# Performance work log

Hardware: AMD Instinct MI355X
Metric: run time of the kernel (lower is better)

## Reference

```python
import jax, jax.numpy as jnp
import numpy as np

TOP_K = 2
NORM_P = 1  # moe_normalize_expert_weights


def setup_inputs() -> dict:
    key = jax.random.key(0)
    k1, k2 = jax.random.split(key)
    B, S, H, E = 4, 4096, 4096, 64
    x = jax.random.normal(k1, (B, S, H), dtype=jnp.float32)
    # Linear(H, E, bias=False) weight, torch layout [E, H]
    W = jax.random.normal(k2, (E, H), dtype=jnp.float32) * (1.0 / np.sqrt(H))
    return {"x": x, "W": W}


def reference(x, W):
    H = x.shape[-1]
    xt = x.reshape(-1, H)                      # [T, H]
    logits = jnp.einsum('th,eh->te', xt, W)    # [T, E]
    scores = jax.nn.softmax(logits, axis=-1)   # [T, E]
    expert_weights, expert_indices = jax.lax.top_k(scores, TOP_K)  # [T, K]
    # p=1 norm over the selected weights (values are positive post-softmax)
    norm = jnp.sum(jnp.abs(expert_weights), axis=-1, keepdims=True)
    expert_weights = expert_weights / norm
    return scores, expert_weights, expert_indices
```

## Files before the change

kernel.cpp:

```cpp
#include <hip/hip_runtime.h>
#include <math.h>

#define TOKS  16384
#define HD    4096
#define NE    64
#define MT    32
#define KT    64
#define NTHR  256
#define NTILE (HD / KT)

typedef unsigned int   u32;
typedef unsigned short u16;
typedef short v8s __attribute__((ext_vector_type(8)));
typedef float v4f __attribute__((ext_vector_type(4)));

__device__ __forceinline__ void split2(float a, float b, u32& hi, u32& lo) {
    u32 ua = __float_as_uint(a), ub = __float_as_uint(b);
    hi = (ub & 0xffff0000u) | (ua >> 16);
    float la = a - __uint_as_float(ua & 0xffff0000u);
    float lb = b - __uint_as_float(ub & 0xffff0000u);
    lo = (__float_as_uint(lb) & 0xffff0000u) | (__float_as_uint(la) >> 16);
}

__global__ __launch_bounds__(256) void wsplit_kernel(const float* __restrict__ W,
                                                     char* __restrict__ wsd) {
    const int gid = blockIdx.x * 256 + threadIdx.x;
    const float4 f = ((const float4*)W)[gid];
    const int idx = gid << 2;
    const int e   = idx >> 12;
    const int col = idx & 4095;
    const int k   = col >> 6;
    const int j   = col & 63;
    u32 h0, h1, l0, l1;
    split2(f.x, f.y, h0, l0);
    split2(f.z, f.w, h1, l1);
    char* base = wsd + ((size_t)k << 14) + (e << 7) + ((j << 1) ^ ((e & 7) << 4));
    *(uint2*)(base)        = make_uint2(h0, h1);
    *(uint2*)(base + 8192) = make_uint2(l0, l1);
}

#define GLDS(G, L)                                                             \
    __builtin_amdgcn_global_load_lds(                                          \
        (const __attribute__((address_space(1))) u32*)(G),                     \
        (__attribute__((address_space(3))) u32*)(L), 16, 0, 0)

__global__ __launch_bounds__(NTHR, 2) void router_kernel(
    const float* __restrict__ x, const char* __restrict__ wsd,
    float* __restrict__ scores, float* __restrict__ wout, float* __restrict__ iout)
{
    __shared__ __align__(16) u16 WT[2][8192];
    __shared__ float Ls[MT][NE + 1];
    __shared__ float Ssum[MT], Smax[MT];

    const int t    = threadIdx.x;
    const int tok0 = blockIdx.x * MT;
    const int lane = t & 63;
    const int w    = t >> 6;
    const int wt   = w & 1;
    const int weh  = w >> 1;
    const int q    = lane >> 4, r = lane & 15;
    const int arow  = wt * 16 + r;
    const int brow0 = weh * 32 + r;
    const int brow1 = weh * 32 + 16 + r;

    const float* xrow = x + (size_t)(tok0 + arow) * HD;
    const int qe = q * 8;

    const int sw0 = (brow0 & 7) << 4;
    const int sw1 = (brow1 & 7) << 4;
    const int ob0h = brow0 * 128, ob0l = 8192 + ob0h;
    const int ob1h = brow1 * 128, ob1l = 8192 + ob1h;
    const int q16 = q * 16;
    const int c00 = ob0h + ((q16)      ^ sw0);
    const int c01 = ob0h + ((64 + q16) ^ sw0);
    const int d00 = ob0l + ((q16)      ^ sw0);
    const int d01 = ob0l + ((64 + q16) ^ sw0);
    const int c10 = ob1h + ((q16)      ^ sw1);
    const int c11 = ob1h + ((64 + q16) ^ sw1);
    const int d10 = ob1l + ((q16)      ^ sw1);
    const int d11 = ob1l + ((64 + q16) ^ sw1);

    const char* wsl = wsd + w * 4096 + lane * 16;

    v4f acc0 = {0.f, 0.f, 0.f, 0.f};
    v4f acc1 = {0.f, 0.f, 0.f, 0.f};

    float4 a0A, a1A, a2A, a3A, a0B, a1B, a2B, a3B;

#define XLOAD(S, T)                                                 \
    do { const float* xp = xrow + (T) * KT + qe;                    \
         a0##S = *(const float4*)(xp);                              \
         a1##S = *(const float4*)(xp + 4);                          \
         a2##S = *(const float4*)(xp + 32);                         \
         a3##S = *(const float4*)(xp + 36); } while (0)

#define STAGE_W(T, B)                                               \
    do { const char* gs = wsl + ((size_t)(T) << 14);                \
         char* ls = ((char*)&WT[B][0]) + w * 4096;                  \
         GLDS(gs,        ls);                                       \
         GLDS(gs + 1024, ls + 1024);                                \
         GLDS(gs + 2048, ls + 2048);                                \
         GLDS(gs + 3072, ls + 3072); } while (0)

#define COMPUTE(S, B)                                                            \
    do {                                                                         \
        const char* WB = (const char*)&WT[B][0];                                 \
        union { v8s v; u32 u[4]; } ah, al;                                       \
        v8s bh0, bl0, bh1, bl1;                                                  \
                                                                      \
        split2(a0##S.x, a0##S.y, ah.u[0], al.u[0]);                              \
        split2(a0##S.z, a0##S.w, ah.u[1], al.u[1]);                              \
        split2(a1##S.x, a1##S.y, ah.u[2], al.u[2]);                              \
        split2(a1##S.z, a1##S.w, ah.u[3], al.u[3]);                              \
        bh0 = *(const v8s*)(WB + c00); bl0 = *(const v8s*)(WB + d00);            \
        bh1 = *(const v8s*)(WB + c10); bl1 = *(const v8s*)(WB + d10);            \
        acc0 = __builtin_amdgcn_mfma_f32_16x16x32_bf16(ah.v, bh0, acc0, 0, 0, 0);\
        acc0 = __builtin_amdgcn_mfma_f32_16x16x32_bf16(al.v, bh0, acc0, 0, 0, 0);\
        acc0 = __builtin_amdgcn_mfma_f32_16x16x32_bf16(ah.v, bl0, acc0, 0, 0, 0);\
        acc1 = __builtin_amdgcn_mfma_f32_16x16x32_bf16(ah.v, bh1, acc1, 0, 0, 0);\
        acc1 = __builtin_amdgcn_mfma_f32_16x16x32_bf16(al.v, bh1, acc1, 0, 0, 0);\
        acc1 = __builtin_amdgcn_mfma_f32_16x16x32_bf16(ah.v, bl1, acc1, 0, 0, 0);\
                                                                      \
        split2(a2##S.x, a2##S.y, ah.u[0], al.u[0]);                              \
        split2(a2##S.z, a2##S.w, ah.u[1], al.u[1]);                              \
        split2(a3##S.x, a3##S.y, ah.u[2], al.u[2]);                              \
        split2(a3##S.z, a3##S.w, ah.u[3], al.u[3]);                              \
        bh0 = *(const v8s*)(WB + c01); bl0 = *(const v8s*)(WB + d01);            \
        bh1 = *(const v8s*)(WB + c11); bl1 = *(const v8s*)(WB + d11);            \
        acc0 = __builtin_amdgcn_mfma_f32_16x16x32_bf16(ah.v, bh0, acc0, 0, 0, 0);\
        acc0 = __builtin_amdgcn_mfma_f32_16x16x32_bf16(al.v, bh0, acc0, 0, 0, 0);\
        acc0 = __builtin_amdgcn_mfma_f32_16x16x32_bf16(ah.v, bl0, acc0, 0, 0, 0);\
        acc1 = __builtin_amdgcn_mfma_f32_16x16x32_bf16(ah.v, bh1, acc1, 0, 0, 0);\
        acc1 = __builtin_amdgcn_mfma_f32_16x16x32_bf16(al.v, bh1, acc1, 0, 0, 0);\
        acc1 = __builtin_amdgcn_mfma_f32_16x16x32_bf16(ah.v, bl1, acc1, 0, 0, 0);\
    } while (0)

    XLOAD(A, 0);
    STAGE_W(0, 0);
    __syncthreads();

    for (int tt = 0; tt < NTILE; tt += 2) {
        STAGE_W(tt + 1, 1);
        XLOAD(B, tt + 1);
        COMPUTE(A, 0);
        __syncthreads();
        if (tt + 2 < NTILE) {
            STAGE_W(tt + 2, 0);
            XLOAD(A, tt + 2);
        }
        COMPUTE(B, 1);
        __syncthreads();
    }

#pragma unroll
    for (int reg = 0; reg < 4; ++reg) {
        Ls[wt * 16 + q * 4 + reg][weh * 32 + r]      = acc0[reg];
        Ls[wt * 16 + q * 4 + reg][weh * 32 + 16 + r] = acc1[reg];
    }
    __syncthreads();

    {
        const int tk = t >> 3;
        const int sl = t & 7;
        float m = -3.402823466e+38f;
#pragma unroll
        for (int j = 0; j < 8; ++j) m = fmaxf(m, Ls[tk][sl + 8 * j]);
#pragma unroll
        for (int d = 1; d < 8; d <<= 1) m = fmaxf(m, __shfl_xor(m, d, 64));

        float s = 0.f, v1 = -1.f, v2 = -1.f;
        int   i1 = 0, i2 = 0;
#pragma unroll
        for (int j = 0; j < 8; ++j) {
            const int e = sl + 8 * j;
            const float ex = expf(Ls[tk][e] - m);
            s += ex;
            if (ex > v1)      { v2 = v1; i2 = i1; v1 = ex; i1 = e; }
            else if (ex > v2) { v2 = ex; i2 = e; }
        }
#pragma unroll
        for (int d = 1; d < 8; d <<= 1) {
            const float ov1 = __shfl_xor(v1, d, 64);
            const int   oi1 = __shfl_xor(i1, d, 64);
            const float ov2 = __shfl_xor(v2, d, 64);
            const int   oi2 = __shfl_xor(i2, d, 64);
            s += __shfl_xor(s, d, 64);
            if (ov1 > v1 || (ov1 == v1 && oi1 < i1)) {
                if (ov2 > v1 || (ov2 == v1 && oi2 < i1)) { v2 = ov2; i2 = oi2; }
                else                                     { v2 = v1;  i2 = i1;  }
                v1 = ov1; i1 = oi1;
            } else if (ov1 > v2 || (ov1 == v2 && oi1 < i2)) {
                v2 = ov1; i2 = oi1;
            }
        }
        if (sl == 0) {
            const float s1 = v1 / s, s2 = v2 / s;
            const float ws_ = s1 + s2;
            wout[(size_t)(tok0 + tk) * 2 + 0] = s1 / ws_;
            wout[(size_t)(tok0 + tk) * 2 + 1] = s2 / ws_;
            iout[(size_t)(tok0 + tk) * 2 + 0] = (float)i1;
            iout[(size_t)(tok0 + tk) * 2 + 1] = (float)i2;
            Ssum[tk] = s;
            Smax[tk] = m;
        }
    }
    __syncthreads();

#pragma unroll
    for (int it = 0; it < (MT * NE) / NTHR; ++it) {
        const int f  = it * NTHR + t;
        const int tk = f >> 6, e = f & 63;
        scores[(size_t)(tok0 + tk) * NE + e] = expf(Ls[tk][e] - Smax[tk]) / Ssum[tk];
    }
}

extern "C" void kernel_launch(void* const* d_in, const int* in_sizes, int n_in,
                              void* d_out, int out_size, void* d_ws, size_t ws_size,
                              hipStream_t stream) {
    (void)in_sizes; (void)n_in; (void)out_size; (void)ws_size;
    const float* x = (const float*)d_in[0];
    const float* W = (const float*)d_in[1];
    float* out    = (float*)d_out;
    float* scores = out;
    float* wout   = scores + (size_t)TOKS * NE;
    float* iout   = wout   + (size_t)TOKS * 2;

    char* wsd = (char*)d_ws;

    wsplit_kernel<<<dim3(256), dim3(256), 0, stream>>>(W, wsd);
    router_kernel<<<dim3(TOKS / MT), dim3(NTHR), 0, stream>>>(x, wsd, scores, wout, iout);
}
```

Before: 398.2 us.

## Deepen router GEMM pipeline to four LDS stages with explicit vmcnt waits

Replaces the double-buffered W staging and x register prefetch with a four-stage ring (three tiles in flight). Instead of a full __syncthreads after each tile, it uses partial s_waitcnt vmcnt counts plus raw barriers, so later loads can stay outstanding while the current tile is computed. This is meant to hide global memory latency in a memory-bound kernel. In exchange it doubles W LDS usage to 64KB and adds 16 more float4 registers per thread, which may lower occupancy at 2 blocks per CU. The hand-counted vmcnt values must also match the compiler's load ordering to stay correct.

```diff
diff --git a/kernel.cpp b/kernel.cpp
--- a/kernel.cpp
+++ b/kernel.cpp
@@ -44,11 +44,17 @@
         (const __attribute__((address_space(1))) u32*)(G),                     \
         (__attribute__((address_space(3))) u32*)(L), 16, 0, 0)
 
+#define VMW16() asm volatile("s_waitcnt vmcnt(16)" ::: "memory")
+#define VMW8()  asm volatile("s_waitcnt vmcnt(8)"  ::: "memory")
+#define VMW0()  asm volatile("s_waitcnt vmcnt(0)"  ::: "memory")
+#define BARR()  do { __builtin_amdgcn_s_barrier();                             \
+                     __builtin_amdgcn_sched_barrier(0); } while (0)
+
 __global__ __launch_bounds__(NTHR, 2) void router_kernel(
     const float* __restrict__ x, const char* __restrict__ wsd,
     float* __restrict__ scores, float* __restrict__ wout, float* __restrict__ iout)
 {
-    __shared__ __align__(16) u16 WT[2][8192];
+    __shared__ __align__(16) u16 WT[4][8192];
     __shared__ float Ls[MT][NE + 1];
     __shared__ float Ssum[MT], Smax[MT];
 
@@ -81,11 +87,13 @@
     const int d11 = ob1l + ((64 + q16) ^ sw1);
 
     const char* wsl = wsd + w * 4096 + lane * 16;
+    char* const wtbase = (char*)&WT[0][0];
 
     v4f acc0 = {0.f, 0.f, 0.f, 0.f};
     v4f acc1 = {0.f, 0.f, 0.f, 0.f};
 
     float4 a0A, a1A, a2A, a3A, a0B, a1B, a2B, a3B;
+    float4 a0C, a1C, a2C, a3C, a0D, a1D, a2D, a3D;
 
 #define XLOAD(S, T)                                                 \
     do { const float* xp = xrow + (T) * KT + qe;                    \
@@ -96,7 +104,7 @@
 
 #define STAGE_W(T, B)                                               \
     do { const char* gs = wsl + ((size_t)(T) << 14);                \
-         char* ls = ((char*)&WT[B][0]) + w * 4096;                  \
+         char* ls = wtbase + (B) * 16384 + w * 4096;                \
          GLDS(gs,        ls);                                       \
          GLDS(gs + 1024, ls + 1024);                                \
          GLDS(gs + 2048, ls + 2048);                                \
@@ -104,7 +112,7 @@
 
 #define COMPUTE(S, B)                                                            \
     do {                                                                         \
-        const char* WB = (const char*)&WT[B][0];                                 \
+        const char* WB = wtbase + (B) * 16384;                                   \
         union { v8s v; u32 u[4]; } ah, al;                                       \
         v8s bh0, bl0, bh1, bl1;                                                  \
                                                                       \
@@ -135,22 +143,33 @@
         acc1 = __builtin_amdgcn_mfma_f32_16x16x32_bf16(ah.v, bl1, acc1, 0, 0, 0);\
     } while (0)
 
-    XLOAD(A, 0);
-    STAGE_W(0, 0);
-    __syncthreads();
-
-    for (int tt = 0; tt < NTILE; tt += 2) {
-        STAGE_W(tt + 1, 1);
-        XLOAD(B, tt + 1);
+    STAGE_W(0, 0); XLOAD(A, 0);
+    STAGE_W(1, 1); XLOAD(B, 1);
+    STAGE_W(2, 2); XLOAD(C, 2);
+
+    for (int tt = 0; tt < 60; tt += 4) {
+        VMW16(); BARR();
+        STAGE_W(tt + 3, 3); XLOAD(D, tt + 3);
         COMPUTE(A, 0);
-        __syncthreads();
-        if (tt + 2 < NTILE) {
-            STAGE_W(tt + 2, 0);
-            XLOAD(A, tt + 2);
-        }
+        VMW16(); BARR();
+        STAGE_W(tt + 4, 0); XLOAD(A, tt + 4);
         COMPUTE(B, 1);
-        __syncthreads();
-    }
+        VMW16(); BARR();
+        STAGE_W(tt + 5, 1); XLOAD(B, tt + 5);
+        COMPUTE(C, 2);
+        VMW16(); BARR();
+        STAGE_W(tt + 6, 2); XLOAD(C, tt + 6);
+        COMPUTE(D, 3);
+    }
+    VMW16(); BARR();
+    STAGE_W(63, 3); XLOAD(D, 63);
+    COMPUTE(A, 0);
+    VMW16(); BARR();
+    COMPUTE(B, 1);
+    VMW8();  BARR();
+    COMPUTE(C, 2);
+    VMW0();  BARR();
+    COMPUTE(D, 3);
 
 #pragma unroll
     for (int reg = 0; reg < 4; ++reg) {
```

Result: no change. 399.8 us (+0.4%).
